# Optimization experiments

Measured on AMD Instinct MI355X. Metric: run time of the kernel, lower is better.

Reference implementation:

```python
import jax, jax.numpy as jnp
import numpy as np

TAU = 2.0
V_TH = 1.0


def setup_inputs() -> dict:
    key = jax.random.key(0)
    k1, k2, k3 = jax.random.split(key, 3)
    T, B, N = 128, 64, 1024
    x = jax.random.normal(k1, (T, B, N), dtype=jnp.float32)
    # nn.Linear(hidden, hidden, bias=False) weights: [out, in]
    scale = 1.0 / np.sqrt(N)
    W1 = jax.random.uniform(k2, (N, N), dtype=jnp.float32, minval=-scale, maxval=scale)
    W2 = jax.random.uniform(k3, (N, N), dtype=jnp.float32, minval=-scale, maxval=scale)
    return {"x": x, "W1": W1, "W2": W2}


def _lif_scan(h_seq):
    # h_seq: [T, B, N]; LIF recurrence with tau=2, v_th=1, reset v = h*(1-s)
    def step(v, x_t):
        h = v + (x_t - v) / TAU
        s = (h >= V_TH).astype(h.dtype)
        return h * (1.0 - s), s

    v0 = jnp.zeros(h_seq.shape[1:], dtype=h_seq.dtype)
    _, spikes = jax.lax.scan(step, v0, h_seq)
    return spikes  # [T, B, N]


def reference(x, W1, W2):
    # fc1: y = x @ W1^T (torch Linear convention)
    h = jnp.einsum('tbn,mn->tbm', x, W1)
    spike = _lif_scan(h)
    return jnp.einsum('tbn,mn->tbm', spike, W2)
```

## Files before the change

kernel.cpp:

```cpp
#include <hip/hip_runtime.h>
#include <hip/hip_bf16.h>
#include <stdint.h>


#define TT 128
#define BB 64
#define NN 1024
#define MROWS (TT * BB)
#define SROW  (BB * NN)
#define MiB   ((size_t)1048576)

typedef _Float16 h8  __attribute__((ext_vector_type(8)));
typedef _Float16 h4v __attribute__((ext_vector_type(4)));
typedef float    f4  __attribute__((ext_vector_type(4)));
typedef float    v2f __attribute__((ext_vector_type(2)));

#if __has_builtin(__builtin_elementwise_fma)
#define V2FMA(a, b, c) __builtin_elementwise_fma((a), (b), (c))
#else
static __device__ __forceinline__ v2f v2fma_(v2f a, v2f b, v2f c) {
    v2f r; r[0] = fmaf(a[0], b[0], c[0]); r[1] = fmaf(a[1], b[1], c[1]); return r;
}
#define V2FMA(a, b, c) v2fma_((a), (b), (c))
#endif

#define GL2LDS(g, l) __builtin_amdgcn_global_load_lds(                         \
    (const __attribute__((address_space(1))) void*)(const void*)(g),           \
    (__attribute__((address_space(3))) void*)(void*)(l), 16, 0, 0)

__global__ __launch_bounds__(256) void prep(const float* __restrict__ W1,
                                            const float* __restrict__ W2,
                                            _Float16* __restrict__ B0, _Float16* __restrict__ B1,
                                            float* __restrict__ W2T) {
    const int nb = blockIdx.x;
    const int tid = threadIdx.x;
    if (nb < 1024) {
        const int i = nb * 256 + tid;
        const float4 v = reinterpret_cast<const float4*>(W1)[i];
        const float f[4] = {v.x, v.y, v.z, v.w};
        h4v a0, a1;
#pragma unroll
        for (int j = 0; j < 4; ++j) {
            const _Float16 c = (_Float16)f[j];
            a0[j] = c;
            a1[j] = (_Float16)((f[j] - (float)c) * 4096.0f);
        }
        reinterpret_cast<h4v*>(B0)[i] = a0;
        reinterpret_cast<h4v*>(B1)[i] = a1;
    } else {
        __shared__ float tile[32][33];
        const int tIdx = nb - 1024;
        const int bx = (tIdx & 31) * 32, by = (tIdx >> 5) * 32;
        const int tx = tid & 31, ty = tid >> 5;
#pragma unroll
        for (int j = 0; j < 32; j += 8)
            tile[ty + j][tx] = W2[(size_t)(by + ty + j) * NN + bx + tx];
        __syncthreads();
#pragma unroll
        for (int j = 0; j < 32; j += 8)
            W2T[(size_t)(bx + ty + j) * NN + by + tx] = tile[tx][ty + j];
    }
}

__global__ __launch_bounds__(256, 2) void gemm_rs(const float* __restrict__ X,
                                                  const _Float16* __restrict__ B0g,
                                                  const _Float16* __restrict__ B1g,
                                                  float* __restrict__ C) {
    __shared__ _Float16 As0[2][4096], As1[2][4096];
    __shared__ _Float16 Bs0[2][4096], Bs1[2][4096];
    const int tid = threadIdx.x, lane = tid & 63, wid = tid >> 6;
    const int wr = wid >> 1, wc = wid & 1;
    const int ib = blockIdx.x;
    const int p  = ((ib >> 6) << 3) + (ib & 7);
    const int cc = (ib >> 3) & 7;
    const int rowBase = p * 128, colBase = cc * 128;

    const int sr = wid * 32 + (lane >> 2);
    const int sc = lane & 3;
    const size_t xOff = (size_t)(rowBase + sr) * NN + sc * 8;
    const int wsw = (sc ^ ((sr >> 1) & 3)) << 3;
    const int wA0 = sr * 32 + wsw;
    const int wA1 = (sr + 16) * 32 + wsw;

    const int swzB = (((lane & 3) ^ ((sr >> 1) & 3)) << 3);
    const size_t bOff0 = (size_t)(colBase + sr) * NN + swzB;
    const size_t bOff1 = bOff0 + (size_t)16 * NN;
    const int l0 = wid * 1024, l1 = l0 + 512;

    int fA[4], fB[4];
#pragma unroll
    for (int i = 0; i < 4; ++i) {
        const int ra = wr * 64 + i * 16 + (lane & 15);
        const int rb = wc * 64 + i * 16 + (lane & 15);
        fA[i] = ra * 32 + (((lane >> 4) ^ ((ra >> 1) & 3)) << 3);
        fB[i] = rb * 32 + (((lane >> 4) ^ ((rb >> 1) & 3)) << 3);
    }

    f4 acc0[4][4], acc1[4][4];
#pragma unroll
    for (int i = 0; i < 4; ++i)
#pragma unroll
        for (int j = 0; j < 4; ++j) { acc0[i][j] = (f4)0.0f; acc1[i][j] = (f4)0.0f; }

    f4 xa0, xa1, xb0, xb1;

#define XLOAD(K0)                                              \
    do {                                                       \
        const size_t xo = xOff + (K0);                         \
        xa0 = *(const f4*)(X + xo);                            \
        xa1 = *(const f4*)(X + xo + 4);                        \
        xb0 = *(const f4*)(X + xo + (size_t)16 * NN);          \
        xb1 = *(const f4*)(X + xo + (size_t)16 * NN + 4);      \
    } while (0)

#define BSTAGE(bi, K0)                                         \
    do {                                                       \
        GL2LDS(B0g + bOff0 + (K0), &Bs0[bi][l0]);              \
        GL2LDS(B0g + bOff1 + (K0), &Bs0[bi][l1]);              \
        GL2LDS(B1g + bOff0 + (K0), &Bs1[bi][l0]);              \
        GL2LDS(B1g + bOff1 + (K0), &Bs1[bi][l1]);              \
    } while (0)

#define AWRITE(bi)                                                             \
    do {                                                                       \
        h8 hi, lo;                                                             \
        _Pragma("unroll") for (int e = 0; e < 4; ++e) {                        \
            const float f0 = xa0[e], f1 = xa1[e];                              \
            const _Float16 c0 = (_Float16)f0, c1 = (_Float16)f1;               \
            hi[e] = c0; hi[4 + e] = c1;                                        \
            lo[e]     = (_Float16)((f0 - (float)c0) * 4096.0f);                \
            lo[4 + e] = (_Float16)((f1 - (float)c1) * 4096.0f);                \
        }                                                                      \
        *(h8*)&As0[bi][wA0] = hi; *(h8*)&As1[bi][wA0] = lo;                    \
        _Pragma("unroll") for (int e = 0; e < 4; ++e) {                        \
            const float f0 = xb0[e], f1 = xb1[e];                              \
            const _Float16 c0 = (_Float16)f0, c1 = (_Float16)f1;               \
            hi[e] = c0; hi[4 + e] = c1;                                        \
            lo[e]     = (_Float16)((f0 - (float)c0) * 4096.0f);                \
            lo[4 + e] = (_Float16)((f1 - (float)c1) * 4096.0f);                \
        }                                                                      \
        *(h8*)&As0[bi][wA1] = hi; *(h8*)&As1[bi][wA1] = lo;                    \
    } while (0)

    XLOAD(0);
    BSTAGE(0, 0);
    AWRITE(0);
    __syncthreads();

    for (int t = 0; t < 32; ++t) {
        const int cur = t & 1;
        if (t < 31) {
            XLOAD((t + 1) * 32);
            BSTAGE(cur ^ 1, (t + 1) * 32);
        }
        h8 a0f[4], a1f[4], b0f[4], b1f[4];
#pragma unroll
        for (int i = 0; i < 4; ++i) {
            a0f[i] = *(const h8*)&As0[cur][fA[i]];
            a1f[i] = *(const h8*)&As1[cur][fA[i]];
            b0f[i] = *(const h8*)&Bs0[cur][fB[i]];
            b1f[i] = *(const h8*)&Bs1[cur][fB[i]];
        }
#pragma unroll
        for (int i = 0; i < 4; ++i)
#pragma unroll
            for (int j = 0; j < 4; ++j) {
                acc0[i][j] = __builtin_amdgcn_mfma_f32_16x16x32_f16(a0f[i], b0f[j], acc0[i][j], 0, 0, 0);
                acc1[i][j] = __builtin_amdgcn_mfma_f32_16x16x32_f16(a0f[i], b1f[j], acc1[i][j], 0, 0, 0);
                acc1[i][j] = __builtin_amdgcn_mfma_f32_16x16x32_f16(a1f[i], b0f[j], acc1[i][j], 0, 0, 0);
            }
        if (t < 31) AWRITE(cur ^ 1);
        __syncthreads();
    }
#undef XLOAD
#undef BSTAGE
#undef AWRITE

    const int orow = rowBase + wr * 64 + (lane >> 4) * 4;
    const int ocol = colBase + wc * 64 + (lane & 15);
#pragma unroll
    for (int i = 0; i < 4; ++i)
#pragma unroll
        for (int j = 0; j < 4; ++j)
#pragma unroll
            for (int q = 0; q < 4; ++q)
                C[(size_t)(orow + i * 16 + q) * NN + ocol + j * 16] =
                    acc0[i][j][q] + acc1[i][j][q] * (1.0f / 4096.0f);
}

__global__ __launch_bounds__(256) void lif_scan(const float* __restrict__ H,
                                                unsigned long long* __restrict__ mask) {
    const int g = blockIdx.x * 256 + threadIdx.x;
    const int b = g >> 10;
    const int n = g & 1023;
    const int word = n >> 6;
    const bool lane0 = (threadIdx.x & 63) == 0;

    float v = 0.0f;
    float buf[16];
#pragma unroll
    for (int j = 0; j < 16; ++j) buf[j] = H[(size_t)j * SROW + g];

    for (int t0 = 0; t0 < TT; t0 += 16) {
        float nbuf[16];
        if (t0 + 16 < TT) {
#pragma unroll
            for (int j = 0; j < 16; ++j) nbuf[j] = H[(size_t)(t0 + 16 + j) * SROW + g];
        } else {
#pragma unroll
            for (int j = 0; j < 16; ++j) nbuf[j] = 0.f;
        }
#pragma unroll
        for (int j = 0; j < 16; ++j) {
            const float x = buf[j];
            const float h = v + (x - v) * 0.5f;
            const bool s = (h >= 1.0f);
            v = s ? 0.0f : h;
            const unsigned long long m = __ballot(s);
            if (lane0) mask[((size_t)(t0 + j) * BB + b) * 16 + word] = m;
        }
#pragma unroll
        for (int j = 0; j < 16; ++j) buf[j] = nbuf[j];
    }
}

__global__ __launch_bounds__(256) void spike_matmul(const unsigned long long* __restrict__ mask,
                                                    const float* __restrict__ W2T,
                                                    float* __restrict__ out) {
    __shared__ unsigned long long sw[16];
    const int r = blockIdx.x;
    const int tid = threadIdx.x;
    if (tid < 16) sw[tid] = mask[(size_t)r * 16 + tid];
    __syncthreads();

    f4 acc = (f4)0.0f;
#pragma unroll 1
    for (int w = 0; w < 16; ++w) {
        unsigned long long bits = sw[w];
        while (bits) {
            const int n = w * 64 + (__ffsll(bits) - 1);
            bits &= bits - 1;
            const f4 rv = reinterpret_cast<const f4*>(W2T + (size_t)n * NN)[tid];
            acc[0] += rv[0]; acc[1] += rv[1]; acc[2] += rv[2]; acc[3] += rv[3];
        }
    }
    reinterpret_cast<f4*>(out + (size_t)r * NN)[tid] = acc;
}

__global__ __launch_bounds__(256) void transpose_nn(const float* __restrict__ in,
                                                    float* __restrict__ out) {
    __shared__ float tile[32][33];
    const int bx = blockIdx.x * 32, by = blockIdx.y * 32;
    const int tx = threadIdx.x, ty = threadIdx.y;
#pragma unroll
    for (int j = 0; j < 32; j += 8)
        tile[ty + j][tx] = in[(size_t)(by + ty + j) * NN + bx + tx];
    __syncthreads();
#pragma unroll
    for (int j = 0; j < 32; j += 8)
        out[(size_t)(bx + ty + j) * NN + by + tx] = tile[tx][ty + j];
}

#define BM 128
#define BN 64
#define BK 16
__global__ __launch_bounds__(256, 4) void gemm1_f32(const float* __restrict__ A,
                                                    const float* __restrict__ B,
                                                    float* __restrict__ C) {
    __shared__ float Asb[2][BK][132];
    __shared__ float Bsb[2][BK][68];
    const int tid = threadIdx.x;
    const int ty = tid >> 4;
    const int tx = tid & 15;
    const int rowBase = blockIdx.y * BM;
    const int colBase = blockIdx.x * BN;
    const int sr = tid >> 2;
    const int sk = (tid & 3) * 4;

    const float* Ap0 = A + (size_t)(rowBase + sr) * NN + sk;
    const float* Ap1 = Ap0 + (size_t)64 * NN;
    const float* Bp  = B + (size_t)(colBase + sr) * NN + sk;

    v2f acc[4][4];
#pragma unroll
    for (int i = 0; i < 4; ++i)
#pragma unroll
        for (int j = 0; j < 4; ++j) acc[i][j] = (v2f){0.f, 0.f};

    float4 ra0 = *(const float4*)Ap0;
    float4 ra1 = *(const float4*)Ap1;
    float4 rb  = *(const float4*)Bp;

#define STW(buf)                                                                       \
    do {                                                                               \
        Asb[buf][sk + 0][sr] = ra0.x; Asb[buf][sk + 1][sr] = ra0.y;                    \
        Asb[buf][sk + 2][sr] = ra0.z; Asb[buf][sk + 3][sr] = ra0.w;                    \
        Asb[buf][sk + 0][sr + 64] = ra1.x; Asb[buf][sk + 1][sr + 64] = ra1.y;          \
        Asb[buf][sk + 2][sr + 64] = ra1.z; Asb[buf][sk + 3][sr + 64] = ra1.w;          \
        Bsb[buf][sk + 0][sr] = rb.x;  Bsb[buf][sk + 1][sr] = rb.y;                     \
        Bsb[buf][sk + 2][sr] = rb.z;  Bsb[buf][sk + 3][sr] = rb.w;                     \
    } while (0)

    STW(0);
    __syncthreads();
    const int NT = NN / BK;
    for (int t = 0; t < NT; ++t) {
        const int cur = t & 1;
        if (t < NT - 1) {
            const int ko = (t + 1) * BK;
            ra0 = *(const float4*)(Ap0 + ko);
            ra1 = *(const float4*)(Ap1 + ko);
            rb  = *(const float4*)(Bp + ko);
        }
#pragma unroll
        for (int k = 0; k < BK; ++k) {
            const v2f* ap = (const v2f*)&Asb[cur][k][ty * 8];
            const float4 bf = *(const float4*)&Bsb[cur][k][tx * 4];
            const float bb[4] = {bf.x, bf.y, bf.z, bf.w};
            const v2f a0 = ap[0], a1 = ap[1], a2 = ap[2], a3 = ap[3];
#pragma unroll
            for (int j = 0; j < 4; ++j) {
                const v2f bd = {bb[j], bb[j]};
                acc[0][j] = V2FMA(a0, bd, acc[0][j]);
                acc[1][j] = V2FMA(a1, bd, acc[1][j]);
                acc[2][j] = V2FMA(a2, bd, acc[2][j]);
                acc[3][j] = V2FMA(a3, bd, acc[3][j]);
            }
        }
        if (t < NT - 1) STW(cur ^ 1);
        __syncthreads();
    }
#undef STW
    float* Cp = C + (size_t)(rowBase + ty * 8) * NN + colBase + tx * 4;
#pragma unroll
    for (int rp = 0; rp < 4; ++rp) {
        float4 lo = {acc[rp][0][0], acc[rp][1][0], acc[rp][2][0], acc[rp][3][0]};
        float4 hi = {acc[rp][0][1], acc[rp][1][1], acc[rp][2][1], acc[rp][3][1]};
        *(float4*)(Cp + (size_t)(2 * rp) * NN)     = lo;
        *(float4*)(Cp + (size_t)(2 * rp + 1) * NN) = hi;
    }
}

extern "C" void kernel_launch(void* const* d_in, const int* in_sizes, int n_in,
                              void* d_out, int out_size, void* d_ws, size_t ws_size,
                              hipStream_t stream) {
    const float* x  = (const float*)d_in[0];
    const float* W1 = (const float*)d_in[1];
    const float* W2 = (const float*)d_in[2];
    float* out = (float*)d_out;

    unsigned long long* mask = (unsigned long long*)d_ws;
    float* W2T = (float*)((char*)d_ws + 1 * MiB);

    if (ws_size >= 9 * MiB) {
        _Float16* B0 = (_Float16*)((char*)d_ws + 5 * MiB);
        _Float16* B1 = (_Float16*)((char*)d_ws + 7 * MiB);

        prep<<<2048, 256, 0, stream>>>(W1, W2, B0, B1, W2T);
        gemm_rs<<<512, 256, 0, stream>>>(x, B0, B1, out);
    } else {
        transpose_nn<<<dim3(32, 32), dim3(32, 8), 0, stream>>>(W2, W2T);
        gemm1_f32<<<dim3(NN / BN, MROWS / BM), 256, 0, stream>>>(x, W1, out);
    }
    lif_scan<<<SROW / 256, 256, 0, stream>>>(out, mask);
    spike_matmul<<<MROWS, 256, 0, stream>>>(mask, W2T, out);
}
```

Before: 164.2 us.

## Fuse W1 split-fp16 conversion and W2 transpose into the first GEMM kernel

Removes the separate prep kernel. W1 is now loaded as fp32 and split into hi/lo fp16 parts inside the GEMM main loop, using the same register-staged path as X instead of async global-to-LDS copies of pre-converted halves. The W2 transpose moves into 64 extra blocks appended to the GEMM grid. This saves one launch and the round trip of the converted W1 through memory. In exchange, every GEMM block redoes the W1 conversion, W1 reads double in bytes, and register and VALU pressure in the inner loop go up.

```diff
diff --git a/kernel.cpp b/kernel.cpp
--- a/kernel.cpp
+++ b/kernel.cpp
@@ -11,7 +11,6 @@
 #define MiB   ((size_t)1048576)
 
 typedef _Float16 h8  __attribute__((ext_vector_type(8)));
-typedef _Float16 h4v __attribute__((ext_vector_type(4)));
 typedef float    f4  __attribute__((ext_vector_type(4)));
 typedef float    v2f __attribute__((ext_vector_type(2)));
 
@@ -24,68 +23,47 @@
 #define V2FMA(a, b, c) v2fma_((a), (b), (c))
 #endif
 
-#define GL2LDS(g, l) __builtin_amdgcn_global_load_lds(                         \
-    (const __attribute__((address_space(1))) void*)(const void*)(g),           \
-    (__attribute__((address_space(3))) void*)(void*)(l), 16, 0, 0)
-
-__global__ __launch_bounds__(256) void prep(const float* __restrict__ W1,
-                                            const float* __restrict__ W2,
-                                            _Float16* __restrict__ B0, _Float16* __restrict__ B1,
-                                            float* __restrict__ W2T) {
-    const int nb = blockIdx.x;
-    const int tid = threadIdx.x;
-    if (nb < 1024) {
-        const int i = nb * 256 + tid;
-        const float4 v = reinterpret_cast<const float4*>(W1)[i];
-        const float f[4] = {v.x, v.y, v.z, v.w};
-        h4v a0, a1;
-#pragma unroll
-        for (int j = 0; j < 4; ++j) {
-            const _Float16 c = (_Float16)f[j];
-            a0[j] = c;
-            a1[j] = (_Float16)((f[j] - (float)c) * 4096.0f);
-        }
-        reinterpret_cast<h4v*>(B0)[i] = a0;
-        reinterpret_cast<h4v*>(B1)[i] = a1;
-    } else {
-        __shared__ float tile[32][33];
-        const int tIdx = nb - 1024;
-        const int bx = (tIdx & 31) * 32, by = (tIdx >> 5) * 32;
-        const int tx = tid & 31, ty = tid >> 5;
-#pragma unroll
-        for (int j = 0; j < 32; j += 8)
-            tile[ty + j][tx] = W2[(size_t)(by + ty + j) * NN + bx + tx];
-        __syncthreads();
-#pragma unroll
-        for (int j = 0; j < 32; j += 8)
-            W2T[(size_t)(bx + ty + j) * NN + by + tx] = tile[tx][ty + j];
-    }
-}
-
-__global__ __launch_bounds__(256, 2) void gemm_rs(const float* __restrict__ X,
-                                                  const _Float16* __restrict__ B0g,
-                                                  const _Float16* __restrict__ B1g,
-                                                  float* __restrict__ C) {
+__global__ __launch_bounds__(256, 2) void gemm_fused(const float* __restrict__ X,
+                                                     const float* __restrict__ W1,
+                                                     const float* __restrict__ W2,
+                                                     float* __restrict__ W2T,
+                                                     float* __restrict__ C) {
     __shared__ _Float16 As0[2][4096], As1[2][4096];
     __shared__ _Float16 Bs0[2][4096], Bs1[2][4096];
     const int tid = threadIdx.x, lane = tid & 63, wid = tid >> 6;
+    const int ib = blockIdx.x;
+
+    if (ib >= 512) {
+        float* tile = (float*)&As0[0][0];
+        const int tx = tid & 31, ty = tid >> 5;
+#pragma unroll 1
+        for (int it = 0; it < 16; ++it) {
+            const int tIdx = (ib - 512) * 16 + it;
+            const int bx = (tIdx & 31) * 32, by = (tIdx >> 5) * 32;
+#pragma unroll
+            for (int j = 0; j < 32; j += 8)
+                tile[(ty + j) * 33 + tx] = W2[(size_t)(by + ty + j) * NN + bx + tx];
+            __syncthreads();
+#pragma unroll
+            for (int j = 0; j < 32; j += 8)
+                W2T[(size_t)(bx + ty + j) * NN + by + tx] = tile[tx * 33 + ty + j];
+            __syncthreads();
+        }
+        return;
+    }
+
     const int wr = wid >> 1, wc = wid & 1;
-    const int ib = blockIdx.x;
     const int p  = ((ib >> 6) << 3) + (ib & 7);
     const int cc = (ib >> 3) & 7;
     const int rowBase = p * 128, colBase = cc * 128;
 
     const int sr = wid * 32 + (lane >> 2);
     const int sc = lane & 3;
+    const int wsw = (sc ^ ((sr >> 1) & 3)) << 3;
+    const int wL0 = sr * 32 + wsw;
+    const int wL1 = (sr + 16) * 32 + wsw;
     const size_t xOff = (size_t)(rowBase + sr) * NN + sc * 8;
-    const int wsw = (sc ^ ((sr >> 1) & 3)) << 3;
-    const int wA0 = sr * 32 + wsw;
-    const int wA1 = (sr + 16) * 32 + wsw;
-
-    const int swzB = (((lane & 3) ^ ((sr >> 1) & 3)) << 3);
-    const size_t bOff0 = (size_t)(colBase + sr) * NN + swzB;
-    const size_t bOff1 = bOff0 + (size_t)16 * NN;
-    const int l0 = wid * 1024, l1 = l0 + 512;
+    const size_t wOff = (size_t)(colBase + sr) * NN + sc * 8;
 
     int fA[4], fB[4];
 #pragma unroll
@@ -103,56 +81,50 @@
         for (int j = 0; j < 4; ++j) { acc0[i][j] = (f4)0.0f; acc1[i][j] = (f4)0.0f; }
 
     f4 xa0, xa1, xb0, xb1;
-
-#define XLOAD(K0)                                              \
+    f4 wa0, wa1, wb0, wb1;
+
+#define LOADS(K0)                                              \
     do {                                                       \
         const size_t xo = xOff + (K0);                         \
         xa0 = *(const f4*)(X + xo);                            \
         xa1 = *(const f4*)(X + xo + 4);                        \
         xb0 = *(const f4*)(X + xo + (size_t)16 * NN);          \
         xb1 = *(const f4*)(X + xo + (size_t)16 * NN + 4);      \
+        const size_t wo = wOff + (K0);                         \
+        wa0 = *(const f4*)(W1 + wo);                           \
+        wa1 = *(const f4*)(W1 + wo + 4);                       \
+        wb0 = *(const f4*)(W1 + wo + (size_t)16 * NN);         \
+        wb1 = *(const f4*)(W1 + wo + (size_t)16 * NN + 4);     \
     } while (0)
 
-#define BSTAGE(bi, K0)                                         \
-    do {                                                       \
-        GL2LDS(B0g + bOff0 + (K0), &Bs0[bi][l0]);              \
-        GL2LDS(B0g + bOff1 + (K0), &Bs0[bi][l1]);              \
-        GL2LDS(B1g + bOff0 + (K0), &Bs1[bi][l0]);              \
-        GL2LDS(B1g + bOff1 + (K0), &Bs1[bi][l1]);              \
-    } while (0)
-
-#define AWRITE(bi)                                                             \
+#define CVTW(S0, S1, D0, D1, OFS)                                              \
     do {                                                                       \
         h8 hi, lo;                                                             \
         _Pragma("unroll") for (int e = 0; e < 4; ++e) {                        \
-            const float f0 = xa0[e], f1 = xa1[e];                              \
+            const float f0 = (S0)[e], f1 = (S1)[e];                            \
             const _Float16 c0 = (_Float16)f0, c1 = (_Float16)f1;               \
             hi[e] = c0; hi[4 + e] = c1;                                        \
             lo[e]     = (_Float16)((f0 - (float)c0) * 4096.0f);                \
             lo[4 + e] = (_Float16)((f1 - (float)c1) * 4096.0f);                \
         }                                                                      \
-        *(h8*)&As0[bi][wA0] = hi; *(h8*)&As1[bi][wA0] = lo;                    \
-        _Pragma("unroll") for (int e = 0; e < 4; ++e) {                        \
-            const float f0 = xb0[e], f1 = xb1[e];                              \
-            const _Float16 c0 = (_Float16)f0, c1 = (_Float16)f1;               \
-            hi[e] = c0; hi[4 + e] = c1;                                        \
-            lo[e]     = (_Float16)((f0 - (float)c0) * 4096.0f);                \
-            lo[4 + e] = (_Float16)((f1 - (float)c1) * 4096.0f);                \
-        }                                                                      \
-        *(h8*)&As0[bi][wA1] = hi; *(h8*)&As1[bi][wA1] = lo;                    \
+        *(h8*)&(D0)[OFS] = hi; *(h8*)&(D1)[OFS] = lo;                          \
     } while (0)
 
-    XLOAD(0);
-    BSTAGE(0, 0);
-    AWRITE(0);
+#define WRITES(bi)                                   \
+    do {                                             \
+        CVTW(xa0, xa1, As0[bi], As1[bi], wL0);       \
+        CVTW(xb0, xb1, As0[bi], As1[bi], wL1);       \
+        CVTW(wa0, wa1, Bs0[bi], Bs1[bi], wL0);       \
+        CVTW(wb0, wb1, Bs0[bi], Bs1[bi], wL1);       \
+    } while (0)
+
+    LOADS(0);
+    WRITES(0);
     __syncthreads();
 
     for (int t = 0; t < 32; ++t) {
         const int cur = t & 1;
-        if (t < 31) {
-            XLOAD((t + 1) * 32);
-            BSTAGE(cur ^ 1, (t + 1) * 32);
-        }
+        if (t < 31) LOADS((t + 1) * 32);
         h8 a0f[4], a1f[4], b0f[4], b1f[4];
 #pragma unroll
         for (int i = 0; i < 4; ++i) {
@@ -169,12 +141,12 @@
                 acc1[i][j] = __builtin_amdgcn_mfma_f32_16x16x32_f16(a0f[i], b1f[j], acc1[i][j], 0, 0, 0);
                 acc1[i][j] = __builtin_amdgcn_mfma_f32_16x16x32_f16(a1f[i], b0f[j], acc1[i][j], 0, 0, 0);
             }
-        if (t < 31) AWRITE(cur ^ 1);
+        if (t < 31) WRITES(cur ^ 1);
         __syncthreads();
     }
-#undef XLOAD
-#undef BSTAGE
-#undef AWRITE
+#undef LOADS
+#undef CVTW
+#undef WRITES
 
     const int orow = rowBase + wr * 64 + (lane >> 4) * 4;
     const int ocol = colBase + wc * 64 + (lane & 15);
@@ -352,12 +324,8 @@
     unsigned long long* mask = (unsigned long long*)d_ws;
     float* W2T = (float*)((char*)d_ws + 1 * MiB);
 
-    if (ws_size >= 9 * MiB) {
-        _Float16* B0 = (_Float16*)((char*)d_ws + 5 * MiB);
-        _Float16* B1 = (_Float16*)((char*)d_ws + 7 * MiB);
-
-        prep<<<2048, 256, 0, stream>>>(W1, W2, B0, B1, W2T);
-        gemm_rs<<<512, 256, 0, stream>>>(x, B0, B1, out);
+    if (ws_size >= 5 * MiB) {
+        gemm_fused<<<576, 256, 0, stream>>>(x, W1, W2, W2T, out);
     } else {
         transpose_nn<<<dim3(32, 32), dim3(32, 8), 0, stream>>>(W2, W2T);
         gemm1_f32<<<dim3(NN / BN, MROWS / BM), 256, 0, stream>>>(x, W1, out);
```

Result: slower. 178.4 us (+8.7%).

## Fuse LIF scan with spike matmul per batch and fold W2 transpose into GEMM

Applied to the files above, without the earlier changes.

Replaces the separate LIF scan and spike-matmul kernels with one kernel of 64 blocks of 1024 threads. Each block scans one batch row over all timesteps, keeps the spike bitmasks in shared memory, then sums the selected W2T rows for each timestep. The W2 transpose moves into 64 extra blocks of the first GEMM launch, and W1 prep gets its own kernel. This removes the global mask round trip and one launch, but cuts the sparse-matmul stage from thousands of blocks to 64. The scalar gather per timestep then runs serially inside each block, which risks poor GPU utilisation and latency-bound loads.

```diff
diff --git a/kernel.cpp b/kernel.cpp
--- a/kernel.cpp
+++ b/kernel.cpp
@@ -28,49 +28,54 @@
     (const __attribute__((address_space(1))) void*)(const void*)(g),           \
     (__attribute__((address_space(3))) void*)(void*)(l), 16, 0, 0)
 
-__global__ __launch_bounds__(256) void prep(const float* __restrict__ W1,
-                                            const float* __restrict__ W2,
-                                            _Float16* __restrict__ B0, _Float16* __restrict__ B1,
-                                            float* __restrict__ W2T) {
-    const int nb = blockIdx.x;
-    const int tid = threadIdx.x;
-    if (nb < 1024) {
-        const int i = nb * 256 + tid;
-        const float4 v = reinterpret_cast<const float4*>(W1)[i];
-        const float f[4] = {v.x, v.y, v.z, v.w};
-        h4v a0, a1;
-#pragma unroll
-        for (int j = 0; j < 4; ++j) {
-            const _Float16 c = (_Float16)f[j];
-            a0[j] = c;
-            a1[j] = (_Float16)((f[j] - (float)c) * 4096.0f);
-        }
-        reinterpret_cast<h4v*>(B0)[i] = a0;
-        reinterpret_cast<h4v*>(B1)[i] = a1;
-    } else {
-        __shared__ float tile[32][33];
-        const int tIdx = nb - 1024;
-        const int bx = (tIdx & 31) * 32, by = (tIdx >> 5) * 32;
-        const int tx = tid & 31, ty = tid >> 5;
-#pragma unroll
-        for (int j = 0; j < 32; j += 8)
-            tile[ty + j][tx] = W2[(size_t)(by + ty + j) * NN + bx + tx];
-        __syncthreads();
-#pragma unroll
-        for (int j = 0; j < 32; j += 8)
-            W2T[(size_t)(bx + ty + j) * NN + by + tx] = tile[tx][ty + j];
-    }
+__global__ __launch_bounds__(256) void prep_w1(const float* __restrict__ W1,
+                                               _Float16* __restrict__ B0,
+                                               _Float16* __restrict__ B1) {
+    const int i = blockIdx.x * 256 + threadIdx.x;
+    const float4 v = reinterpret_cast<const float4*>(W1)[i];
+    const float f[4] = {v.x, v.y, v.z, v.w};
+    h4v a0, a1;
+#pragma unroll
+    for (int j = 0; j < 4; ++j) {
+        const _Float16 c = (_Float16)f[j];
+        a0[j] = c;
+        a1[j] = (_Float16)((f[j] - (float)c) * 4096.0f);
+    }
+    reinterpret_cast<h4v*>(B0)[i] = a0;
+    reinterpret_cast<h4v*>(B1)[i] = a1;
 }
 
 __global__ __launch_bounds__(256, 2) void gemm_rs(const float* __restrict__ X,
                                                   const _Float16* __restrict__ B0g,
                                                   const _Float16* __restrict__ B1g,
+                                                  const float* __restrict__ W2,
+                                                  float* __restrict__ W2T,
                                                   float* __restrict__ C) {
     __shared__ _Float16 As0[2][4096], As1[2][4096];
     __shared__ _Float16 Bs0[2][4096], Bs1[2][4096];
     const int tid = threadIdx.x, lane = tid & 63, wid = tid >> 6;
+    const int ib = blockIdx.x;
+
+    if (ib >= 512) {
+        float* tile = (float*)&As0[0][0];
+        const int tx = tid & 31, ty = tid >> 5;
+#pragma unroll 1
+        for (int it = 0; it < 16; ++it) {
+            const int tIdx = (ib - 512) * 16 + it;
+            const int bx = (tIdx & 31) * 32, by = (tIdx >> 5) * 32;
+#pragma unroll
+            for (int j = 0; j < 32; j += 8)
+                tile[(ty + j) * 33 + tx] = W2[(size_t)(by + ty + j) * NN + bx + tx];
+            __syncthreads();
+#pragma unroll
+            for (int j = 0; j < 32; j += 8)
+                W2T[(size_t)(bx + ty + j) * NN + by + tx] = tile[tx * 33 + ty + j];
+            __syncthreads();
+        }
+        return;
+    }
+
     const int wr = wid >> 1, wc = wid & 1;
-    const int ib = blockIdx.x;
     const int p  = ((ib >> 6) << 3) + (ib & 7);
     const int cc = (ib >> 3) & 7;
     const int rowBase = p * 128, colBase = cc * 128;
@@ -188,24 +193,26 @@
                     acc0[i][j][q] + acc1[i][j][q] * (1.0f / 4096.0f);
 }
 
-__global__ __launch_bounds__(256) void lif_scan(const float* __restrict__ H,
-                                                unsigned long long* __restrict__ mask) {
-    const int g = blockIdx.x * 256 + threadIdx.x;
-    const int b = g >> 10;
-    const int n = g & 1023;
-    const int word = n >> 6;
-    const bool lane0 = (threadIdx.x & 63) == 0;
-
+__global__ __launch_bounds__(1024) void scan_spmm(const float* __restrict__ H,
+                                                  const float* __restrict__ W2T,
+                                                  float* __restrict__ out) {
+    __shared__ unsigned long long msk[TT * 16];
+    const int b = blockIdx.x;
+    const int tid = threadIdx.x;
+    const int w = tid >> 6;
+    const bool lane0 = (tid & 63) == 0;
+
+    const float* Hb = H + (size_t)b * NN + tid;
     float v = 0.0f;
     float buf[16];
 #pragma unroll
-    for (int j = 0; j < 16; ++j) buf[j] = H[(size_t)j * SROW + g];
+    for (int j = 0; j < 16; ++j) buf[j] = Hb[(size_t)j * SROW];
 
     for (int t0 = 0; t0 < TT; t0 += 16) {
         float nbuf[16];
         if (t0 + 16 < TT) {
 #pragma unroll
-            for (int j = 0; j < 16; ++j) nbuf[j] = H[(size_t)(t0 + 16 + j) * SROW + g];
+            for (int j = 0; j < 16; ++j) nbuf[j] = Hb[(size_t)(t0 + 16 + j) * SROW];
         } else {
 #pragma unroll
             for (int j = 0; j < 16; ++j) nbuf[j] = 0.f;
@@ -217,34 +224,27 @@
             const bool s = (h >= 1.0f);
             v = s ? 0.0f : h;
             const unsigned long long m = __ballot(s);
-            if (lane0) mask[((size_t)(t0 + j) * BB + b) * 16 + word] = m;
+            if (lane0) msk[(t0 + j) * 16 + w] = m;
         }
 #pragma unroll
         for (int j = 0; j < 16; ++j) buf[j] = nbuf[j];
     }
-}
-
-__global__ __launch_bounds__(256) void spike_matmul(const unsigned long long* __restrict__ mask,
-                                                    const float* __restrict__ W2T,
-                                                    float* __restrict__ out) {
-    __shared__ unsigned long long sw[16];
-    const int r = blockIdx.x;
-    const int tid = threadIdx.x;
-    if (tid < 16) sw[tid] = mask[(size_t)r * 16 + tid];
     __syncthreads();
 
-    f4 acc = (f4)0.0f;
 #pragma unroll 1
-    for (int w = 0; w < 16; ++w) {
-        unsigned long long bits = sw[w];
-        while (bits) {
-            const int n = w * 64 + (__ffsll(bits) - 1);
-            bits &= bits - 1;
-            const f4 rv = reinterpret_cast<const f4*>(W2T + (size_t)n * NN)[tid];
-            acc[0] += rv[0]; acc[1] += rv[1]; acc[2] += rv[2]; acc[3] += rv[3];
-        }
-    }
-    reinterpret_cast<f4*>(out + (size_t)r * NN)[tid] = acc;
+    for (int t = 0; t < TT; ++t) {
+        float acc = 0.f;
+#pragma unroll 1
+        for (int ww = 0; ww < 16; ++ww) {
+            unsigned long long bits = msk[t * 16 + ww];
+            while (bits) {
+                const int n2 = ww * 64 + (__ffsll(bits) - 1);
+                bits &= bits - 1;
+                acc += W2T[(size_t)n2 * NN + tid];
+            }
+        }
+        out[((size_t)t * BB + b) * NN + tid] = acc;
+    }
 }
 
 __global__ __launch_bounds__(256) void transpose_nn(const float* __restrict__ in,
@@ -349,19 +349,17 @@
     const float* W2 = (const float*)d_in[2];
     float* out = (float*)d_out;
 
-    unsigned long long* mask = (unsigned long long*)d_ws;
-    float* W2T = (float*)((char*)d_ws + 1 * MiB);
-
-    if (ws_size >= 9 * MiB) {
-        _Float16* B0 = (_Float16*)((char*)d_ws + 5 * MiB);
-        _Float16* B1 = (_Float16*)((char*)d_ws + 7 * MiB);
-
-        prep<<<2048, 256, 0, stream>>>(W1, W2, B0, B1, W2T);
-        gemm_rs<<<512, 256, 0, stream>>>(x, B0, B1, out);
+    float* W2T = (float*)d_ws;
+
+    if (ws_size >= 8 * MiB) {
+        _Float16* B0 = (_Float16*)((char*)d_ws + 4 * MiB);
+        _Float16* B1 = (_Float16*)((char*)d_ws + 6 * MiB);
+
+        prep_w1<<<1024, 256, 0, stream>>>(W1, B0, B1);
+        gemm_rs<<<576, 256, 0, stream>>>(x, B0, B1, W2, W2T, out);
     } else {
         transpose_nn<<<dim3(32, 32), dim3(32, 8), 0, stream>>>(W2, W2T);
         gemm1_f32<<<dim3(NN / BN, MROWS / BM), 256, 0, stream>>>(x, W1, out);
     }
-    lif_scan<<<SROW / 256, 256, 0, stream>>>(out, mask);
-    spike_matmul<<<MROWS, 256, 0, stream>>>(mask, W2T, out);
-}
+    scan_spmm<<<BB, 1024, 0, stream>>>(out, W2T, out);
+}
```

New measurement: 335.9 us. +104.6%, slower.
